# Optimization experiments

Hardware: AMD Instinct MI355X
Metric: run time of the kernel (lower is better)

The kernel has to match this reference:

```python
import jax, jax.numpy as jnp
import numpy as np

N = 100000      # nodes
E = 1600000     # edges (avg degree 16)
DIN = 128       # input feature dim
DOUT = 64       # per-head output dim
H = 4           # independent heads, mean-aggregated
LRELU_ALPHA = 0.2  # tf.nn.leaky_relu default


def setup_inputs() -> dict:
    key = jax.random.key(0)
    k = jax.random.split(key, 7)
    inputs = jax.random.normal(k[0], (N, DIN), dtype=jnp.float32)
    edge_row = jnp.sort(jax.random.randint(k[1], (E,), 0, N, dtype=jnp.int32))
    edge_col = jax.random.randint(k[2], (E,), 0, N, dtype=jnp.int32)
    edge_val = jnp.ones((E,), dtype=jnp.float32)  # binary adjacency values
    # Glorot-ish scaled params per head
    W = jax.random.normal(k[3], (H, DIN, DOUT), dtype=jnp.float32) * np.float32(1.0 / np.sqrt(DIN))
    a1 = jax.random.normal(k[4], (H, DOUT), dtype=jnp.float32) * np.float32(1.0 / np.sqrt(DOUT))
    a2 = jax.random.normal(k[5], (H, DOUT), dtype=jnp.float32) * np.float32(1.0 / np.sqrt(DOUT))
    b = jnp.zeros((H, DOUT), dtype=jnp.float32)  # contrib.layers.bias_add bias
    return {"inputs": inputs, "W": W, "a1": a1, "a2": a2, "b": b,
            "edge_val": edge_val, "edge_row": edge_row, "edge_col": edge_col}


def _gat_head(inputs, Wh, a1h, a2h, bh, edge_val, edge_row, edge_col):
    xh = inputs @ Wh                          # [N, DOUT]  per-head projection
    f1 = jax.nn.elu(xh @ a1h)                 # [N]  Dense(D,1, act=elu) on key=x
    f2 = jax.nn.elu(xh @ a2h)                 # [N]
    # sparse_add of adj*f1 (row-broadcast) and adj*f2^T (col-broadcast)
    le = jax.nn.leaky_relu(edge_val * (f1[edge_row] + f2[edge_col]), LRELU_ALPHA)  # [E]
    # sparse softmax per destination row (reverse_axis=1)
    m = jax.ops.segment_max(le, edge_row, num_segments=N)        # [N]
    ex = jnp.exp(le - m[edge_row])                               # [E]
    s = jax.ops.segment_sum(ex, edge_row, num_segments=N)        # [N]
    coef = ex / s[edge_row]                                      # [E]
    # sparse_dense_matmul: out[r] = sum_e coef_e * x[col_e]
    out = jax.ops.segment_sum(coef[:, None] * xh[edge_col], edge_row, num_segments=N)  # [N, DOUT]
    return jax.nn.elu(out + bh)


def reference(inputs, W, a1, a2, b, edge_val, edge_row, edge_col):
    res = jnp.zeros((N, DOUT), dtype=inputs.dtype)
    for h in range(H):  # small fixed head count; each head has independent weights
        res = res + _gat_head(inputs, W[h], a1[h], a2[h], b[h], edge_val, edge_row, edge_col)
    return res / H
```

## Files before the change

kernel.cpp:

```cpp
#include <hip/hip_runtime.h>

#define NN 100000
#define EE 1600000
#define DIN 128
#define DOUT 64
#define NH 4

typedef __attribute__((ext_vector_type(8))) short bf16x8;
typedef __attribute__((ext_vector_type(4))) float f32x4;

__device__ __forceinline__ float elu_f(float x) {
  return x > 0.f ? x : (__expf(x) - 1.f);
}
__device__ __forceinline__ float lrelu_f(float x) {
  return x > 0.f ? x : 0.2f * x;
}
__device__ __forceinline__ float b2f(unsigned short u) {
  union { unsigned int i; float f; } v; v.i = ((unsigned int)u) << 16; return v.f;
}
__device__ __forceinline__ unsigned short f2b(float f) {
  union { float f; unsigned int i; } v; v.f = f;
  unsigned int r = v.i + 0x7fffu + ((v.i >> 16) & 1u);
  return (unsigned short)(r >> 16);
}

__global__ __launch_bounds__(256) void wbf_k(
    const float* __restrict__ W, unsigned short* __restrict__ wbt) {
  int idx = blockIdx.x * 256 + threadIdx.x;
  int col = idx >> 7, k = idx & 127;
  int h = col >> 6, j = col & 63;
  wbt[idx] = f2b(W[(size_t)h * DIN * DOUT + k * DOUT + j]);
}

__global__ __launch_bounds__(256) void build_row_ptr_k(
    const int* __restrict__ erow, int* __restrict__ rp) {
  int r = blockIdx.x * 256 + threadIdx.x;
  if (r > NN) return;
  int lo = 0, hi = EE;
  while (lo < hi) {
    int mid = (lo + hi) >> 1;
    if (erow[mid] < r) lo = mid + 1; else hi = mid;
  }
  rp[r] = lo;
}

__global__ __launch_bounds__(256) void proj_mfma_k(
    const float* __restrict__ inp, const unsigned short* __restrict__ wbt,
    const float* __restrict__ a1, const float* __restrict__ a2,
    float* __restrict__ f1p, float* __restrict__ f2p,
    unsigned short* __restrict__ xh) {
  __shared__ unsigned short lds_a[64 * 128];
  const int tid = threadIdx.x;
  const int h = tid >> 6;
  const int l = tid & 63;
  const int lr = l & 15;
  const int lk = l >> 4;
  const int row0 = blockIdx.x * 64;

  #pragma unroll
  for (int i = 0; i < 8; ++i) {
    const int idx = i * 256 + tid;
    const int row = idx >> 5;
    const int c4 = idx & 31;
    int grow = row0 + row;
    if (grow >= NN) grow = NN - 1;
    const float4 v = *(const float4*)(inp + (size_t)grow * DIN + c4 * 4);
    ushort4 w;
    w.x = f2b(v.x); w.y = f2b(v.y); w.z = f2b(v.z); w.w = f2b(v.w);
    const int byte_off = row * 256 + ((c4 * 8) ^ ((row & 7) << 4));
    *(ushort4*)((char*)lds_a + byte_off) = w;
  }

  bf16x8 bf[4][4];
  #pragma unroll
  for (int n = 0; n < 4; ++n) {
    const int col = h * DOUT + n * 16 + lr;
    #pragma unroll
    for (int kc = 0; kc < 4; ++kc)
      bf[n][kc] = *(const bf16x8*)(wbt + (size_t)col * DIN + kc * 32 + lk * 8);
  }
  __syncthreads();

  f32x4 acc[4][4];
  #pragma unroll
  for (int m = 0; m < 4; ++m)
    #pragma unroll
    for (int n = 0; n < 4; ++n)
      acc[m][n] = (f32x4)(0.f);

  #pragma unroll
  for (int m = 0; m < 4; ++m) {
    const int r = m * 16 + lr;
    bf16x8 af[4];
    #pragma unroll
    for (int kc = 0; kc < 4; ++kc)
      af[kc] = *(const bf16x8*)((char*)lds_a + r * 256 +
                                ((kc * 64 + lk * 16) ^ ((r & 7) << 4)));
    #pragma unroll
    for (int kc = 0; kc < 4; ++kc)
      #pragma unroll
      for (int n = 0; n < 4; ++n)
        acc[m][n] = __builtin_amdgcn_mfma_f32_16x16x32_bf16(
            bf[n][kc], af[kc], acc[m][n], 0, 0, 0);
  }

  float4 a1q[4], a2q[4];
  #pragma unroll
  for (int n = 0; n < 4; ++n) {
    a1q[n] = *(const float4*)(a1 + h * DOUT + n * 16 + lk * 4);
    a2q[n] = *(const float4*)(a2 + h * DOUT + n * 16 + lk * 4);
  }
  #pragma unroll
  for (int m = 0; m < 4; ++m) {
    const int row = row0 + m * 16 + lr;
    const bool ok = row < NN;
    float p1 = 0.f, p2 = 0.f;
    #pragma unroll
    for (int n = 0; n < 4; ++n) {
      const f32x4 a = acc[m][n];
      ushort4 pk;
      pk.x = f2b(a[0]); pk.y = f2b(a[1]); pk.z = f2b(a[2]); pk.w = f2b(a[3]);
      if (ok)
        *(ushort4*)(xh + (size_t)row * (NH * DOUT) + h * DOUT + n * 16 + lk * 4) = pk;
      p1 = fmaf(a[0], a1q[n].x, p1); p1 = fmaf(a[1], a1q[n].y, p1);
      p1 = fmaf(a[2], a1q[n].z, p1); p1 = fmaf(a[3], a1q[n].w, p1);
      p2 = fmaf(a[0], a2q[n].x, p2); p2 = fmaf(a[1], a2q[n].y, p2);
      p2 = fmaf(a[2], a2q[n].z, p2); p2 = fmaf(a[3], a2q[n].w, p2);
    }
    p1 += __shfl_xor(p1, 16); p1 += __shfl_xor(p1, 32);
    p2 += __shfl_xor(p2, 16); p2 += __shfl_xor(p2, 32);
    if (ok && lk == 0) {
      f1p[(size_t)row * NH + h] = elu_f(p1);
      f2p[(size_t)row * NH + h] = elu_f(p2);
    }
  }
}

__global__ __launch_bounds__(256) void agg_k(
    const int* __restrict__ rp, const int* __restrict__ ecol,
    const float* __restrict__ eval, const float* __restrict__ f1p,
    const float* __restrict__ f2p, const unsigned short* __restrict__ xh,
    const float* __restrict__ b, float* __restrict__ out) {
  const int tid = threadIdx.x;
  const int wave = tid >> 6, lane = tid & 63;
  const int r = blockIdx.x * 4 + wave;
  if (r >= NN) return;
  const int g = lane >> 4;
  int e0 = __builtin_amdgcn_readfirstlane(rp[r]);
  int e1 = __builtin_amdgcn_readfirstlane(rp[r + 1]);
  const float f1r = f1p[(size_t)r * NH + g];
  float ax = 0.f, ay = 0.f, az = 0.f, aw = 0.f;
  float ssum = 0.f;
  int e = e0;
  for (; e + 8 <= e1; e += 8) {
    int c[8]; float vv[8];
    #pragma unroll
    for (int u = 0; u < 8; ++u) { c[u] = ecol[e + u]; vv[u] = eval[e + u]; }
    ushort4 xv[8]; float f2v[8];
    #pragma unroll
    for (int u = 0; u < 8; ++u) {
      xv[u] = *(const ushort4*)(xh + (size_t)c[u] * (NH * DOUT) + lane * 4);
      f2v[u] = f2p[(size_t)c[u] * NH + g];
    }
    #pragma unroll
    for (int u = 0; u < 8; ++u) {
      const float ex = __expf(lrelu_f(vv[u] * (f1r + f2v[u])));
      ssum += ex;
      ax = fmaf(ex, b2f(xv[u].x), ax);
      ay = fmaf(ex, b2f(xv[u].y), ay);
      az = fmaf(ex, b2f(xv[u].z), az);
      aw = fmaf(ex, b2f(xv[u].w), aw);
    }
  }
  if (e < e1) {
    int c[8]; float vv[8]; bool okk[8];
    #pragma unroll
    for (int u = 0; u < 8; ++u) {
      int ee = e + u;
      okk[u] = ee < e1;
      if (!okk[u]) ee = e1 - 1;
      c[u] = ecol[ee]; vv[u] = eval[ee];
    }
    ushort4 xv[8]; float f2v[8];
    #pragma unroll
    for (int u = 0; u < 8; ++u) {
      xv[u] = *(const ushort4*)(xh + (size_t)c[u] * (NH * DOUT) + lane * 4);
      f2v[u] = f2p[(size_t)c[u] * NH + g];
    }
    #pragma unroll
    for (int u = 0; u < 8; ++u) {
      float ex = __expf(lrelu_f(vv[u] * (f1r + f2v[u])));
      ex = okk[u] ? ex : 0.f;
      ssum += ex;
      ax = fmaf(ex, b2f(xv[u].x), ax);
      ay = fmaf(ex, b2f(xv[u].y), ay);
      az = fmaf(ex, b2f(xv[u].z), az);
      aw = fmaf(ex, b2f(xv[u].w), aw);
    }
  }
  const float4 bb = *(const float4*)(b + lane * 4);
  const float inv = (e1 > e0) ? (1.f / ssum) : 0.f;
  float v0 = elu_f(ax * inv + bb.x);
  float v1 = elu_f(ay * inv + bb.y);
  float v2 = elu_f(az * inv + bb.z);
  float v3 = elu_f(aw * inv + bb.w);
  v0 += __shfl_xor(v0, 16); v1 += __shfl_xor(v1, 16);
  v2 += __shfl_xor(v2, 16); v3 += __shfl_xor(v3, 16);
  v0 += __shfl_xor(v0, 32); v1 += __shfl_xor(v1, 32);
  v2 += __shfl_xor(v2, 32); v3 += __shfl_xor(v3, 32);
  if (lane < 16) {
    f32x4 o = {v0 * 0.25f, v1 * 0.25f, v2 * 0.25f, v3 * 0.25f};
    __builtin_nontemporal_store(o, (f32x4*)(out + (size_t)r * DOUT + lane * 4));
  }
}

extern "C" void kernel_launch(void* const* d_in, const int* in_sizes, int n_in,
                              void* d_out, int out_size, void* d_ws, size_t ws_size,
                              hipStream_t stream) {
  const float* inp = (const float*)d_in[0];
  const float* W   = (const float*)d_in[1];
  const float* a1  = (const float*)d_in[2];
  const float* a2  = (const float*)d_in[3];
  const float* b   = (const float*)d_in[4];
  const float* ev  = (const float*)d_in[5];
  const int* erow  = (const int*)d_in[6];
  const int* ecol  = (const int*)d_in[7];
  float* out = (float*)d_out;

  char* ws = (char*)d_ws;
  size_t off = 0;
  int* rp = (int*)(ws + off);
  off += (((size_t)(NN + 1) * 4) + 255) & ~(size_t)255;
  float* f1p = (float*)(ws + off);
  off += (((size_t)NH * NN * 4) + 255) & ~(size_t)255;
  float* f2p = (float*)(ws + off);
  off += (((size_t)NH * NN * 4) + 255) & ~(size_t)255;
  unsigned short* xh = (unsigned short*)(ws + off);
  off += (((size_t)NN * NH * DOUT * 2) + 255) & ~(size_t)255;
  unsigned short* wbt = (unsigned short*)(ws + off);

  wbf_k<<<(NH * DIN * DOUT) / 256, 256, 0, stream>>>(W, wbt);
  build_row_ptr_k<<<(NN + 1 + 255) / 256, 256, 0, stream>>>(erow, rp);
  proj_mfma_k<<<(NN + 63) / 64, 256, 0, stream>>>(inp, wbt, a1, a2, f1p, f2p, xh);
  agg_k<<<(NN + 3) / 4, 256, 0, stream>>>(rp, ecol, ev, f1p, f2p, xh, b, out);
}
```

Before: 177.2 us.

## Merge prep kernels, use persistent aggregation grid, stream weight fragments per k-chunk

```diff
diff --git a/kernel.cpp b/kernel.cpp
--- a/kernel.cpp
+++ b/kernel.cpp
@@ -5,15 +5,13 @@
 #define DIN 128
 #define DOUT 64
 #define NH 4
+#define AGG_BLOCKS 2048
 
 typedef __attribute__((ext_vector_type(8))) short bf16x8;
 typedef __attribute__((ext_vector_type(4))) float f32x4;
 
 __device__ __forceinline__ float elu_f(float x) {
   return x > 0.f ? x : (__expf(x) - 1.f);
-}
-__device__ __forceinline__ float lrelu_f(float x) {
-  return x > 0.f ? x : 0.2f * x;
 }
 __device__ __forceinline__ float b2f(unsigned short u) {
   union { unsigned int i; float f; } v; v.i = ((unsigned int)u) << 16; return v.f;
@@ -24,24 +22,23 @@
   return (unsigned short)(r >> 16);
 }
 
-__global__ __launch_bounds__(256) void wbf_k(
-    const float* __restrict__ W, unsigned short* __restrict__ wbt) {
-  int idx = blockIdx.x * 256 + threadIdx.x;
-  int col = idx >> 7, k = idx & 127;
-  int h = col >> 6, j = col & 63;
-  wbt[idx] = f2b(W[(size_t)h * DIN * DOUT + k * DOUT + j]);
-}
-
-__global__ __launch_bounds__(256) void build_row_ptr_k(
+__global__ __launch_bounds__(256) void prep_k(
+    const float* __restrict__ W, unsigned short* __restrict__ wbt,
     const int* __restrict__ erow, int* __restrict__ rp) {
-  int r = blockIdx.x * 256 + threadIdx.x;
-  if (r > NN) return;
-  int lo = 0, hi = EE;
-  while (lo < hi) {
-    int mid = (lo + hi) >> 1;
-    if (erow[mid] < r) lo = mid + 1; else hi = mid;
-  }
-  rp[r] = lo;
+  const int gid = blockIdx.x * 256 + threadIdx.x;
+  if (gid < NH * DIN * DOUT) {
+    int col = gid >> 7, k = gid & 127;
+    int h = col >> 6, j = col & 63;
+    wbt[gid] = f2b(W[(size_t)h * DIN * DOUT + k * DOUT + j]);
+  }
+  if (gid <= NN) {
+    int lo = 0, hi = EE;
+    while (lo < hi) {
+      int mid = (lo + hi) >> 1;
+      if (erow[mid] < gid) lo = mid + 1; else hi = mid;
+    }
+    rp[gid] = lo;
+  }
 }
 
 __global__ __launch_bounds__(256) void proj_mfma_k(
@@ -70,15 +67,6 @@
     const int byte_off = row * 256 + ((c4 * 8) ^ ((row & 7) << 4));
     *(ushort4*)((char*)lds_a + byte_off) = w;
   }
-
-  bf16x8 bf[4][4];
-  #pragma unroll
-  for (int n = 0; n < 4; ++n) {
-    const int col = h * DOUT + n * 16 + lr;
-    #pragma unroll
-    for (int kc = 0; kc < 4; ++kc)
-      bf[n][kc] = *(const bf16x8*)(wbt + (size_t)col * DIN + kc * 32 + lk * 8);
-  }
   __syncthreads();
 
   f32x4 acc[4][4];
@@ -89,19 +77,22 @@
       acc[m][n] = (f32x4)(0.f);
 
   #pragma unroll
-  for (int m = 0; m < 4; ++m) {
-    const int r = m * 16 + lr;
-    bf16x8 af[4];
-    #pragma unroll
-    for (int kc = 0; kc < 4; ++kc)
-      af[kc] = *(const bf16x8*)((char*)lds_a + r * 256 +
-                                ((kc * 64 + lk * 16) ^ ((r & 7) << 4)));
-    #pragma unroll
-    for (int kc = 0; kc < 4; ++kc)
+  for (int kc = 0; kc < 4; ++kc) {
+    bf16x8 bfn[4];
+    #pragma unroll
+    for (int n = 0; n < 4; ++n)
+      bfn[n] = *(const bf16x8*)(wbt + (size_t)(h * DOUT + n * 16 + lr) * DIN +
+                                kc * 32 + lk * 8);
+    #pragma unroll
+    for (int m = 0; m < 4; ++m) {
+      const int r = m * 16 + lr;
+      const bf16x8 af = *(const bf16x8*)((char*)lds_a + r * 256 +
+                                         ((kc * 64 + lk * 16) ^ ((r & 7) << 4)));
       #pragma unroll
       for (int n = 0; n < 4; ++n)
         acc[m][n] = __builtin_amdgcn_mfma_f32_16x16x32_bf16(
-            bf[n][kc], af[kc], acc[m][n], 0, 0, 0);
+            bfn[n], af, acc[m][n], 0, 0, 0);
+    }
   }
 
   float4 a1q[4], a2q[4];
@@ -143,74 +134,78 @@
     const float* __restrict__ b, float* __restrict__ out) {
   const int tid = threadIdx.x;
   const int wave = tid >> 6, lane = tid & 63;
-  const int r = blockIdx.x * 4 + wave;
-  if (r >= NN) return;
+  const int wid0 = blockIdx.x * 4 + wave;
   const int g = lane >> 4;
-  int e0 = __builtin_amdgcn_readfirstlane(rp[r]);
-  int e1 = __builtin_amdgcn_readfirstlane(rp[r + 1]);
-  const float f1r = f1p[(size_t)r * NH + g];
-  float ax = 0.f, ay = 0.f, az = 0.f, aw = 0.f;
-  float ssum = 0.f;
-  int e = e0;
-  for (; e + 8 <= e1; e += 8) {
-    int c[8]; float vv[8];
-    #pragma unroll
-    for (int u = 0; u < 8; ++u) { c[u] = ecol[e + u]; vv[u] = eval[e + u]; }
-    ushort4 xv[8]; float f2v[8];
-    #pragma unroll
-    for (int u = 0; u < 8; ++u) {
-      xv[u] = *(const ushort4*)(xh + (size_t)c[u] * (NH * DOUT) + lane * 4);
-      f2v[u] = f2p[(size_t)c[u] * NH + g];
-    }
-    #pragma unroll
-    for (int u = 0; u < 8; ++u) {
-      const float ex = __expf(lrelu_f(vv[u] * (f1r + f2v[u])));
-      ssum += ex;
-      ax = fmaf(ex, b2f(xv[u].x), ax);
-      ay = fmaf(ex, b2f(xv[u].y), ay);
-      az = fmaf(ex, b2f(xv[u].z), az);
-      aw = fmaf(ex, b2f(xv[u].w), aw);
-    }
-  }
-  if (e < e1) {
-    int c[8]; float vv[8]; bool okk[8];
-    #pragma unroll
-    for (int u = 0; u < 8; ++u) {
-      int ee = e + u;
-      okk[u] = ee < e1;
-      if (!okk[u]) ee = e1 - 1;
-      c[u] = ecol[ee]; vv[u] = eval[ee];
-    }
-    ushort4 xv[8]; float f2v[8];
-    #pragma unroll
-    for (int u = 0; u < 8; ++u) {
-      xv[u] = *(const ushort4*)(xh + (size_t)c[u] * (NH * DOUT) + lane * 4);
-      f2v[u] = f2p[(size_t)c[u] * NH + g];
-    }
-    #pragma unroll
-    for (int u = 0; u < 8; ++u) {
-      float ex = __expf(lrelu_f(vv[u] * (f1r + f2v[u])));
-      ex = okk[u] ? ex : 0.f;
-      ssum += ex;
-      ax = fmaf(ex, b2f(xv[u].x), ax);
-      ay = fmaf(ex, b2f(xv[u].y), ay);
-      az = fmaf(ex, b2f(xv[u].z), az);
-      aw = fmaf(ex, b2f(xv[u].w), aw);
-    }
-  }
   const float4 bb = *(const float4*)(b + lane * 4);
-  const float inv = (e1 > e0) ? (1.f / ssum) : 0.f;
-  float v0 = elu_f(ax * inv + bb.x);
-  float v1 = elu_f(ay * inv + bb.y);
-  float v2 = elu_f(az * inv + bb.z);
-  float v3 = elu_f(aw * inv + bb.w);
-  v0 += __shfl_xor(v0, 16); v1 += __shfl_xor(v1, 16);
-  v2 += __shfl_xor(v2, 16); v3 += __shfl_xor(v3, 16);
-  v0 += __shfl_xor(v0, 32); v1 += __shfl_xor(v1, 32);
-  v2 += __shfl_xor(v2, 32); v3 += __shfl_xor(v3, 32);
-  if (lane < 16) {
-    f32x4 o = {v0 * 0.25f, v1 * 0.25f, v2 * 0.25f, v3 * 0.25f};
-    __builtin_nontemporal_store(o, (f32x4*)(out + (size_t)r * DOUT + lane * 4));
+
+  for (int r = wid0; r < NN; r += 4 * AGG_BLOCKS) {
+    const int e0 = __builtin_amdgcn_readfirstlane(rp[r]);
+    const int e1 = __builtin_amdgcn_readfirstlane(rp[r + 1]);
+    const float f1r = f1p[(size_t)r * NH + g];
+    float ax = 0.f, ay = 0.f, az = 0.f, aw = 0.f;
+    float ssum = 0.f;
+    int e = e0;
+    for (; e + 8 <= e1; e += 8) {
+      int c[8]; float vv[8];
+      #pragma unroll
+      for (int u = 0; u < 8; ++u) { c[u] = ecol[e + u]; vv[u] = eval[e + u]; }
+      ushort4 xv[8]; float f2v[8];
+      #pragma unroll
+      for (int u = 0; u < 8; ++u) {
+        xv[u] = *(const ushort4*)(xh + (size_t)c[u] * (NH * DOUT) + lane * 4);
+        f2v[u] = f2p[(size_t)c[u] * NH + g];
+      }
+      #pragma unroll
+      for (int u = 0; u < 8; ++u) {
+        const float t = vv[u] * (f1r + f2v[u]);
+        const float ex = __expf(fmaxf(t, 0.2f * t));
+        ssum += ex;
+        ax = fmaf(ex, b2f(xv[u].x), ax);
+        ay = fmaf(ex, b2f(xv[u].y), ay);
+        az = fmaf(ex, b2f(xv[u].z), az);
+        aw = fmaf(ex, b2f(xv[u].w), aw);
+      }
+    }
+    if (e < e1) {
+      int c[8]; float vv[8]; bool okk[8];
+      #pragma unroll
+      for (int u = 0; u < 8; ++u) {
+        int ee = e + u;
+        okk[u] = ee < e1;
+        if (!okk[u]) ee = e1 - 1;
+        c[u] = ecol[ee]; vv[u] = eval[ee];
+      }
+      ushort4 xv[8]; float f2v[8];
+      #pragma unroll
+      for (int u = 0; u < 8; ++u) {
+        xv[u] = *(const ushort4*)(xh + (size_t)c[u] * (NH * DOUT) + lane * 4);
+        f2v[u] = f2p[(size_t)c[u] * NH + g];
+      }
+      #pragma unroll
+      for (int u = 0; u < 8; ++u) {
+        const float t = vv[u] * (f1r + f2v[u]);
+        float ex = __expf(fmaxf(t, 0.2f * t));
+        ex = okk[u] ? ex : 0.f;
+        ssum += ex;
+        ax = fmaf(ex, b2f(xv[u].x), ax);
+        ay = fmaf(ex, b2f(xv[u].y), ay);
+        az = fmaf(ex, b2f(xv[u].z), az);
+        aw = fmaf(ex, b2f(xv[u].w), aw);
+      }
+    }
+    const float inv = (e1 > e0) ? (1.f / ssum) : 0.f;
+    float v0 = elu_f(ax * inv + bb.x);
+    float v1 = elu_f(ay * inv + bb.y);
+    float v2 = elu_f(az * inv + bb.z);
+    float v3 = elu_f(aw * inv + bb.w);
+    v0 += __shfl_xor(v0, 16); v1 += __shfl_xor(v1, 16);
+    v2 += __shfl_xor(v2, 16); v3 += __shfl_xor(v3, 16);
+    v0 += __shfl_xor(v0, 32); v1 += __shfl_xor(v1, 32);
+    v2 += __shfl_xor(v2, 32); v3 += __shfl_xor(v3, 32);
+    if (lane < 16) {
+      f32x4 o = {v0 * 0.25f, v1 * 0.25f, v2 * 0.25f, v3 * 0.25f};
+      __builtin_nontemporal_store(o, (f32x4*)(out + (size_t)r * DOUT + lane * 4));
+    }
   }
 }
 
@@ -239,8 +234,7 @@
   off += (((size_t)NN * NH * DOUT * 2) + 255) & ~(size_t)255;
   unsigned short* wbt = (unsigned short*)(ws + off);
 
-  wbf_k<<<(NH * DIN * DOUT) / 256, 256, 0, stream>>>(W, wbt);
-  build_row_ptr_k<<<(NN + 1 + 255) / 256, 256, 0, stream>>>(erow, rp);
+  prep_k<<<(NN + 1 + 255) / 256, 256, 0, stream>>>(W, wbt, erow, rp);
   proj_mfma_k<<<(NN + 63) / 64, 256, 0, stream>>>(inp, wbt, a1, a2, f1p, f2p, xh);
-  agg_k<<<(NN + 3) / 4, 256, 0, stream>>>(rp, ecol, ev, f1p, f2p, xh, b, out);
-}
+  agg_k<<<AGG_BLOCKS, 256, 0, stream>>>(rp, ecol, ev, f1p, f2p, xh, b, out);
+}
```

New measurement: 189.3 us. 6.8% more time.
